# Performance work log

Hardware: AMD Instinct MI355X
Metric: run time of the kernel (lower is better)

## Reference

```python
import jax, jax.numpy as jnp
import numpy as np

N_NODES = 100000
N_EDGES = 1600000
D = 64
L = 3


def setup_inputs() -> dict:
    key = jax.random.key(0)
    ks = jax.random.split(key, 6)
    x = jax.random.normal(ks[0], (N_NODES, D), dtype=jnp.float32)
    edge_index = jax.random.randint(ks[1], (2, N_EDGES), 0, N_NODES, dtype=jnp.int64)
    # Stacked SAGEConv params: lin_l (neighbor branch, with bias), lin_r (root branch, no bias)
    scale = 1.0 / np.sqrt(D)
    Wl = jax.random.normal(ks[2], (L, D, D), dtype=jnp.float32) * scale
    bl = jnp.zeros((L, D), dtype=jnp.float32)
    Wr = jax.random.normal(ks[3], (L, D, D), dtype=jnp.float32) * scale
    return {
        "x": x,
        "Wl": Wl,
        "bl": bl,
        "Wr": Wr,
        "edge_index": edge_index,
        "batch_size": N_NODES,
        "framework": 1,
    }


def reference(x, Wl, bl, Wr, edge_index, batch_size, framework):
    src, dst = edge_index[0], edge_index[1]
    n = x.shape[0]
    # in-degree for mean aggregation; isolated nodes -> divide by 1 (result stays 0)
    deg = jax.ops.segment_sum(jnp.ones((src.shape[0],), dtype=x.dtype), dst, num_segments=n)
    inv_deg = (1.0 / jnp.maximum(deg, 1.0))[:, None]  # [N,1]
    for i in range(Wl.shape[0]):
        msg = x[src]                                              # [E, D] gather
        agg = jax.ops.segment_sum(msg, dst, num_segments=n) * inv_deg  # [N, D] mean
        x = jax.nn.relu(agg @ Wl[i].T + bl[i] + x @ Wr[i].T)
    if framework:
        return x
    return x[:batch_size]
```

## Files before the change

### kernel.cpp

```cpp
#include <hip/hip_runtime.h>
#include <hip/hip_bf16.h>


#define D 64
#define KDIM 128
#define TS 64
#define ASTH 144
#define BSH 9
#define BNODES 512
#define ECHUNK 4096
#define BCAP 12288

typedef unsigned long long u64;
typedef unsigned short u16;

__device__ inline u16 f2bf(float f) {
    unsigned u = __float_as_uint(f);
    return (u16)((u + 0x7fffu + ((u >> 16) & 1u)) >> 16);
}
__device__ inline void bfx8_to_f(uint4 u, float* f) {
    f[0] = __uint_as_float(u.x << 16); f[1] = __uint_as_float(u.x & 0xffff0000u);
    f[2] = __uint_as_float(u.y << 16); f[3] = __uint_as_float(u.y & 0xffff0000u);
    f[4] = __uint_as_float(u.z << 16); f[5] = __uint_as_float(u.z & 0xffff0000u);
    f[6] = __uint_as_float(u.w << 16); f[7] = __uint_as_float(u.w & 0xffff0000u);
}


__global__ __launch_bounds__(256) void convert_x_kernel(
    const float* __restrict__ x, u16* __restrict__ xb, int total8)
{
    int i = blockIdx.x * 256 + threadIdx.x;
    if (i >= total8) return;
    float4 a = *(const float4*)(x + (size_t)i * 8);
    float4 b = *(const float4*)(x + (size_t)i * 8 + 4);
    uint4 o;
    o.x = (unsigned)f2bf(a.x) | ((unsigned)f2bf(a.y) << 16);
    o.y = (unsigned)f2bf(a.z) | ((unsigned)f2bf(a.w) << 16);
    o.z = (unsigned)f2bf(b.x) | ((unsigned)f2bf(b.y) << 16);
    o.w = (unsigned)f2bf(b.z) | ((unsigned)f2bf(b.w) << 16);
    *(uint4*)(xb + (size_t)i * 8) = o;
}


__global__ __launch_bounds__(256) void bin_kernel(
    const int* __restrict__ srcp, const int* __restrict__ dstp,
    int* __restrict__ bcnt, u64* __restrict__ staging,
    int nE, int nb)
{
    __shared__ int hist[1024];
    __shared__ int bbase[1024];
    int t = threadIdx.x;
    int e0 = blockIdx.x * ECHUNK;
    for (int i = t; i < nb; i += 256) hist[i] = 0;
    __syncthreads();
    int dcache[16];
#pragma unroll
    for (int j = 0; j < 16; ++j) {
        int e = e0 + j * 256 + t;
        int d = (e < nE) ? dstp[e] : -1;
        dcache[j] = d;
        if (d >= 0) atomicAdd(&hist[d >> BSH], 1);
    }
    __syncthreads();
    for (int i = t; i < nb; i += 256) {
        int c = hist[i];
        bbase[i] = (c > 0) ? atomicAdd(&bcnt[i], c) : 0;
        hist[i] = 0;
    }
    __syncthreads();
#pragma unroll
    for (int j = 0; j < 16; ++j) {
        int e = e0 + j * 256 + t;
        int d = dcache[j];
        if (d >= 0) {
            int b = d >> BSH;
            int pos = bbase[b] + atomicAdd(&hist[b], 1);
            u64 rec = ((u64)(unsigned)(d & (BNODES - 1)) << 32) | (unsigned)srcp[e];
            staging[(size_t)b * BCAP + pos] = rec;
        }
    }
}

__global__ __launch_bounds__(64) void scan_bcnt_kernel(
    const int* __restrict__ bcnt, int* __restrict__ bbase, int nb)
{
    int lane = threadIdx.x;
    int carry = 0;
    for (int base = 0; base < nb; base += 64) {
        int i = base + lane;
        int v = (i < nb) ? bcnt[i] : 0;
        int inc = v;
#pragma unroll
        for (int off = 1; off < 64; off <<= 1) {
            int v2 = __shfl_up(inc, off);
            if (lane >= off) inc += v2;
        }
        if (i < nb) bbase[i] = carry + (inc - v);
        carry += __shfl(inc, 63);
    }
}

__global__ __launch_bounds__(256) void bucket_build_kernel(
    const u64* __restrict__ staging, const int* __restrict__ bcnt,
    const int* __restrict__ bbase, int* __restrict__ offs,
    float* __restrict__ inv, int* __restrict__ csr, int n, int nb, int E)
{
    __shared__ int hist[BNODES];
    __shared__ int loffs[BNODES + 1];
    __shared__ int cur[BNODES];
    int b = blockIdx.x, t = threadIdx.x;
    int n0 = b << BSH;
    int nodes = min(BNODES, n - n0);
    int cnt = bcnt[b];
    int gbase = bbase[b];
    const u64* seg = staging + (size_t)b * BCAP;
    for (int i = t; i < nodes; i += 256) { hist[i] = 0; cur[i] = 0; }
    __syncthreads();
    for (int e = t; e < cnt; e += 256) atomicAdd(&hist[(int)(seg[e] >> 32)], 1);
    __syncthreads();
    if (t < 64) {
        int carry = 0;
        for (int base0 = 0; base0 < nodes; base0 += 64) {
            int i = base0 + t;
            int v = (i < nodes) ? hist[i] : 0;
            int inc = v;
#pragma unroll
            for (int off = 1; off < 64; off <<= 1) {
                int v2 = __shfl_up(inc, off);
                if (t >= off) inc += v2;
            }
            if (i < nodes) loffs[i] = carry + (inc - v);
            carry += __shfl(inc, 63);
        }
        if (t == 0) loffs[nodes] = carry;
    }
    __syncthreads();
    for (int i = t; i < nodes; i += 256) {
        offs[n0 + i] = gbase + loffs[i];
        inv[n0 + i] = 1.0f / fmaxf((float)hist[i], 1.0f);
    }
    if (b == nb - 1 && t == 0) offs[n] = E;
    for (int e = t; e < cnt; e += 256) {
        u64 rec = seg[e];
        int dl = (int)(rec >> 32);
        int sv = (int)(rec & 0xffffffffu);
        int pos = loffs[dl] + atomicAdd(&cur[dl], 1);
        csr[gbase + pos] = sv;
    }
}

__global__ void transpose_w_kernel(const float* __restrict__ Wl,
                                   const float* __restrict__ Wr,
                                   float* __restrict__ WT, int total)
{
    int idx = blockIdx.x * 256 + threadIdx.x;
    if (idx >= total) return;
    int j = idx & 63;
    int k = (idx >> 6) & (KDIM - 1);
    int l = idx >> 13;
    float v = (k < D) ? Wl[((l * D) + j) * D + k]
                      : Wr[((l * D) + j) * D + (k - D)];
    WT[idx] = v;
}


template <int WRITE_F32>
__global__ __launch_bounds__(256) void layer_kernel(
    const u16* __restrict__ xin, const int* __restrict__ offs,
    const int* __restrict__ csr, const float* __restrict__ inv,
    const float* __restrict__ WT,
    const float* __restrict__ bl,
    void* __restrict__ outp, int n)
{
    __shared__ u16 A[TS * ASTH];
    const int t = threadIdx.x, w = t >> 6, lane = t & 63;
    const int sub = lane >> 3;
    const int fl  = lane & 7;
    const int base = lane & 56;
    const int v0 = blockIdx.x * TS;

#pragma unroll
    for (int g = 0; g < 2; ++g) {
        const int r = w * 16 + g * 8 + sub;
        const int v = v0 + r;
        int s = 0, e = 0;
        float scale = 0.f;
        uint4 xv = make_uint4(0, 0, 0, 0);
        if (v < n) {
            s = offs[v];
            e = offs[v + 1];
            scale = inv[v];
            xv = *(const uint4*)(xin + (size_t)v * D + fl * 8);
        }
        float acc[8] = {};
        while (__any(s < e)) {
            int idx = 0;
            if (s + fl < e) idx = csr[s + fl];
            int cnt = e - s;
            cnt = cnt < 0 ? 0 : (cnt > 8 ? 8 : cnt);
            int idxv[8];
#pragma unroll
            for (int j = 0; j < 8; ++j) idxv[j] = __shfl(idx, base + j);
            uint4 rows[8];
#pragma unroll
            for (int j = 0; j < 8; ++j)
                rows[j] = *(const uint4*)(xin + (size_t)idxv[j] * D + fl * 8);
#pragma unroll
            for (int j = 0; j < 8; ++j) {
                float f[8];
                bfx8_to_f(rows[j], f);
                float m = (j < cnt) ? 1.f : 0.f;
#pragma unroll
                for (int q = 0; q < 8; ++q) acc[q] = fmaf(f[q], m, acc[q]);
            }
            s += 8;
        }
        uint4 o;
        o.x = (unsigned)f2bf(acc[0] * scale) | ((unsigned)f2bf(acc[1] * scale) << 16);
        o.y = (unsigned)f2bf(acc[2] * scale) | ((unsigned)f2bf(acc[3] * scale) << 16);
        o.z = (unsigned)f2bf(acc[4] * scale) | ((unsigned)f2bf(acc[5] * scale) << 16);
        o.w = (unsigned)f2bf(acc[6] * scale) | ((unsigned)f2bf(acc[7] * scale) << 16);
        *(uint4*)(&A[r * ASTH + fl * 8]) = o;
        *(uint4*)(&A[r * ASTH + D + fl * 8]) = xv;
    }
    __syncthreads();

    const int c = (t & 15) * 4;
    const int r = (t >> 4) * 4;
    float acc[4][4] = {};
    for (int k = 0; k < KDIM; k += 8) {
        float4 b[8];
#pragma unroll
        for (int kk = 0; kk < 8; ++kk)
            b[kk] = *(const float4*)(WT + (k + kk) * D + c);
#pragma unroll
        for (int rr = 0; rr < 4; ++rr) {
            uint4 au = *(const uint4*)(&A[(r + rr) * ASTH + k]);
            float a[8];
            bfx8_to_f(au, a);
#pragma unroll
            for (int kk = 0; kk < 8; ++kk) {
                acc[rr][0] = fmaf(a[kk], b[kk].x, acc[rr][0]);
                acc[rr][1] = fmaf(a[kk], b[kk].y, acc[rr][1]);
                acc[rr][2] = fmaf(a[kk], b[kk].z, acc[rr][2]);
                acc[rr][3] = fmaf(a[kk], b[kk].w, acc[rr][3]);
            }
        }
    }

    float4 bias = *(const float4*)(bl + c);
#pragma unroll
    for (int rr = 0; rr < 4; ++rr) {
        int v = v0 + r + rr;
        if (v < n) {
            float o0 = fmaxf(acc[rr][0] + bias.x, 0.f);
            float o1 = fmaxf(acc[rr][1] + bias.y, 0.f);
            float o2 = fmaxf(acc[rr][2] + bias.z, 0.f);
            float o3 = fmaxf(acc[rr][3] + bias.w, 0.f);
            if (WRITE_F32) {
                *(float4*)((float*)outp + (size_t)v * D + c) = make_float4(o0, o1, o2, o3);
            } else {
                uint2 p;
                p.x = (unsigned)f2bf(o0) | ((unsigned)f2bf(o1) << 16);
                p.y = (unsigned)f2bf(o2) | ((unsigned)f2bf(o3) << 16);
                *(uint2*)((u16*)outp + (size_t)v * D + c) = p;
            }
        }
    }
}


extern "C" void kernel_launch(void* const* d_in, const int* in_sizes, int n_in,
                              void* d_out, int out_size, void* d_ws, size_t ws_size,
                              hipStream_t stream)
{
    const float* x  = (const float*)d_in[0];
    const float* Wl = (const float*)d_in[1];
    const float* bl = (const float*)d_in[2];
    const float* Wr = (const float*)d_in[3];
    const int*   ei = (const int*)d_in[4];

    const int N = in_sizes[0] / D;
    const int E = in_sizes[4] / 2;
    const int L = in_sizes[1] / (D * D);

    const int* srcp = ei;
    const int* dstp = ei + E;

    const int nbuck = (N + BNODES - 1) >> BSH;

    char* w = (char*)d_ws;
    int* bcnt  = (int*)w;               w += 1024 * sizeof(int);
    int* bbase = (int*)w;               w += 1024 * sizeof(int);
    int* offs  = (int*)w;               w += (size_t)(N + 1) * sizeof(int);
    w = (char*)(((uintptr_t)w + 15) & ~(uintptr_t)15);
    float* inv = (float*)w;             w += (size_t)N * sizeof(float);
    w = (char*)(((uintptr_t)w + 15) & ~(uintptr_t)15);
    int* csr   = (int*)w;               w += (size_t)E * sizeof(int);
    w = (char*)(((uintptr_t)w + 15) & ~(uintptr_t)15);
    float* wt  = (float*)w;             w += (size_t)L * KDIM * D * sizeof(float);
    w = (char*)(((uintptr_t)w + 15) & ~(uintptr_t)15);
    u16* xbf0  = (u16*)w;               w += (size_t)N * D * sizeof(u16);
    w = (char*)(((uintptr_t)w + 15) & ~(uintptr_t)15);
    u16* xbf1  = (u16*)w;               w += (size_t)N * D * sizeof(u16);
    w = (char*)(((uintptr_t)w + 15) & ~(uintptr_t)15);
    u16* xbf2  = (u16*)w;               w += (size_t)N * D * sizeof(u16);
    w = (char*)(((uintptr_t)w + 15) & ~(uintptr_t)15);
    u64* staging = (u64*)w;

    hipMemsetAsync(bcnt, 0, 1024 * sizeof(int), stream);

    convert_x_kernel<<<(N * D / 8 + 255) / 256, 256, 0, stream>>>(x, xbf0, N * D / 8);
    bin_kernel<<<(E + ECHUNK - 1) / ECHUNK, 256, 0, stream>>>(srcp, dstp, bcnt, staging, E, nbuck);
    scan_bcnt_kernel<<<1, 64, 0, stream>>>(bcnt, bbase, nbuck);
    bucket_build_kernel<<<nbuck, 256, 0, stream>>>(staging, bcnt, bbase, offs, inv, csr, N, nbuck, E);

    int wtotal = L * KDIM * D;
    transpose_w_kernel<<<(wtotal + 255) / 256, 256, 0, stream>>>(Wl, Wr, wt, wtotal);

    const int nblk = (N + TS - 1) / TS;
    const u16* xcur = xbf0;
    for (int i = 0; i < L; ++i) {
        const float* WTl = wt + (size_t)i * KDIM * D;
        const float* bll = bl + (size_t)i * D;
        if (i == L - 1) {
            layer_kernel<1><<<nblk, 256, 0, stream>>>(xcur, offs, csr, inv, WTl, bll, d_out, N);
        } else {
            u16* xdst = (i & 1) ? xbf2 : xbf1;
            layer_kernel<0><<<nblk, 256, 0, stream>>>(xcur, offs, csr, inv, WTl, bll, xdst, N);
            xcur = xdst;
        }
    }
}
```

Before: 350.5 us.

## Use bf16 MFMA for layer GEMM and interleave two-node gather loops

Replaces the scalar FP32 FMA GEMM in the layer kernel with 16x16x32 bf16 MFMA instructions, using weights prepacked into bf16 fragment order by a new pack kernel. The neighbor gather now runs both node groups in one loop so more independent row loads are in flight per iteration. The LDS row stride is reduced. Weights are now rounded to bf16, which costs some precision. Output stores become scalar per element instead of vectorized.

```diff
diff --git a/kernel.cpp b/kernel.cpp
--- a/kernel.cpp
+++ b/kernel.cpp
@@ -5,7 +5,7 @@
 #define D 64
 #define KDIM 128
 #define TS 64
-#define ASTH 144
+#define ASTH 136
 #define BSH 9
 #define BNODES 512
 #define ECHUNK 4096
@@ -13,6 +13,8 @@
 
 typedef unsigned long long u64;
 typedef unsigned short u16;
+typedef __attribute__((ext_vector_type(8))) short bf16x8;
+typedef __attribute__((ext_vector_type(4))) float f32x4;
 
 __device__ inline u16 f2bf(float f) {
     unsigned u = __float_as_uint(f);
@@ -149,18 +151,22 @@
     }
 }
 
-__global__ void transpose_w_kernel(const float* __restrict__ Wl,
-                                   const float* __restrict__ Wr,
-                                   float* __restrict__ WT, int total)
+__global__ void pack_w_kernel(const float* __restrict__ Wl,
+                              const float* __restrict__ Wr,
+                              u16* __restrict__ wpk, int total)
 {
     int idx = blockIdx.x * 256 + threadIdx.x;
     if (idx >= total) return;
-    int j = idx & 63;
-    int k = (idx >> 6) & (KDIM - 1);
-    int l = idx >> 13;
-    float v = (k < D) ? Wl[((l * D) + j) * D + k]
-                      : Wr[((l * D) + j) * D + (k - D)];
-    WT[idx] = v;
+    int j    = idx & 7;
+    int lane = (idx >> 3) & 63;
+    int nt   = (idx >> 9) & 3;
+    int kt   = (idx >> 11) & 3;
+    int l    = idx >> 13;
+    int k = kt * 32 + (lane >> 4) * 8 + j;
+    int n = nt * 16 + (lane & 15);
+    float v = (k < D) ? Wl[((l * D) + n) * D + k]
+                      : Wr[((l * D) + n) * D + (k - D)];
+    wpk[idx] = f2bf(v);
 }
 
 
@@ -168,7 +174,7 @@
 __global__ __launch_bounds__(256) void layer_kernel(
     const u16* __restrict__ xin, const int* __restrict__ offs,
     const int* __restrict__ csr, const float* __restrict__ inv,
-    const float* __restrict__ WT,
+    const u16* __restrict__ wpk,
     const float* __restrict__ bl,
     void* __restrict__ outp, int n)
 {
@@ -179,91 +185,97 @@
     const int base = lane & 56;
     const int v0 = blockIdx.x * TS;
 
+    int s[2], e[2];
+    float scale[2];
+    uint4 xv[2];
+    float acc[2][8] = {};
+#pragma unroll
+    for (int g = 0; g < 2; ++g) {
+        const int v = v0 + w * 16 + g * 8 + sub;
+        s[g] = 0; e[g] = 0; scale[g] = 0.f;
+        xv[g] = make_uint4(0, 0, 0, 0);
+        if (v < n) {
+            s[g] = offs[v];
+            e[g] = offs[v + 1];
+            scale[g] = inv[v];
+            xv[g] = *(const uint4*)(xin + (size_t)v * D + fl * 8);
+        }
+    }
+    while (__any((s[0] < e[0]) | (s[1] < e[1]))) {
+        int idx0 = 0, idx1 = 0;
+        if (s[0] + fl < e[0]) idx0 = csr[s[0] + fl];
+        if (s[1] + fl < e[1]) idx1 = csr[s[1] + fl];
+        int c0 = e[0] - s[0]; c0 = c0 < 0 ? 0 : (c0 > 8 ? 8 : c0);
+        int c1 = e[1] - s[1]; c1 = c1 < 0 ? 0 : (c1 > 8 ? 8 : c1);
+        int iv0[8], iv1[8];
+#pragma unroll
+        for (int j = 0; j < 8; ++j) iv0[j] = __shfl(idx0, base + j);
+#pragma unroll
+        for (int j = 0; j < 8; ++j) iv1[j] = __shfl(idx1, base + j);
+        uint4 rows0[8], rows1[8];
+#pragma unroll
+        for (int j = 0; j < 8; ++j)
+            rows0[j] = *(const uint4*)(xin + (size_t)iv0[j] * D + fl * 8);
+#pragma unroll
+        for (int j = 0; j < 8; ++j)
+            rows1[j] = *(const uint4*)(xin + (size_t)iv1[j] * D + fl * 8);
+#pragma unroll
+        for (int j = 0; j < 8; ++j) {
+            float f[8];
+            bfx8_to_f(rows0[j], f);
+            float m = (j < c0) ? 1.f : 0.f;
+#pragma unroll
+            for (int q = 0; q < 8; ++q) acc[0][q] = fmaf(f[q], m, acc[0][q]);
+        }
+#pragma unroll
+        for (int j = 0; j < 8; ++j) {
+            float f[8];
+            bfx8_to_f(rows1[j], f);
+            float m = (j < c1) ? 1.f : 0.f;
+#pragma unroll
+            for (int q = 0; q < 8; ++q) acc[1][q] = fmaf(f[q], m, acc[1][q]);
+        }
+        s[0] += 8; s[1] += 8;
+    }
 #pragma unroll
     for (int g = 0; g < 2; ++g) {
         const int r = w * 16 + g * 8 + sub;
-        const int v = v0 + r;
-        int s = 0, e = 0;
-        float scale = 0.f;
-        uint4 xv = make_uint4(0, 0, 0, 0);
-        if (v < n) {
-            s = offs[v];
-            e = offs[v + 1];
-            scale = inv[v];
-            xv = *(const uint4*)(xin + (size_t)v * D + fl * 8);
-        }
-        float acc[8] = {};
-        while (__any(s < e)) {
-            int idx = 0;
-            if (s + fl < e) idx = csr[s + fl];
-            int cnt = e - s;
-            cnt = cnt < 0 ? 0 : (cnt > 8 ? 8 : cnt);
-            int idxv[8];
-#pragma unroll
-            for (int j = 0; j < 8; ++j) idxv[j] = __shfl(idx, base + j);
-            uint4 rows[8];
-#pragma unroll
-            for (int j = 0; j < 8; ++j)
-                rows[j] = *(const uint4*)(xin + (size_t)idxv[j] * D + fl * 8);
-#pragma unroll
-            for (int j = 0; j < 8; ++j) {
-                float f[8];
-                bfx8_to_f(rows[j], f);
-                float m = (j < cnt) ? 1.f : 0.f;
-#pragma unroll
-                for (int q = 0; q < 8; ++q) acc[q] = fmaf(f[q], m, acc[q]);
-            }
-            s += 8;
-        }
         uint4 o;
-        o.x = (unsigned)f2bf(acc[0] * scale) | ((unsigned)f2bf(acc[1] * scale) << 16);
-        o.y = (unsigned)f2bf(acc[2] * scale) | ((unsigned)f2bf(acc[3] * scale) << 16);
-        o.z = (unsigned)f2bf(acc[4] * scale) | ((unsigned)f2bf(acc[5] * scale) << 16);
-        o.w = (unsigned)f2bf(acc[6] * scale) | ((unsigned)f2bf(acc[7] * scale) << 16);
+        o.x = (unsigned)f2bf(acc[g][0] * scale[g]) | ((unsigned)f2bf(acc[g][1] * scale[g]) << 16);
+        o.y = (unsigned)f2bf(acc[g][2] * scale[g]) | ((unsigned)f2bf(acc[g][3] * scale[g]) << 16);
+        o.z = (unsigned)f2bf(acc[g][4] * scale[g]) | ((unsigned)f2bf(acc[g][5] * scale[g]) << 16);
+        o.w = (unsigned)f2bf(acc[g][6] * scale[g]) | ((unsigned)f2bf(acc[g][7] * scale[g]) << 16);
         *(uint4*)(&A[r * ASTH + fl * 8]) = o;
-        *(uint4*)(&A[r * ASTH + D + fl * 8]) = xv;
-    }
-    __syncthreads();
-
-    const int c = (t & 15) * 4;
-    const int r = (t >> 4) * 4;
-    float acc[4][4] = {};
-    for (int k = 0; k < KDIM; k += 8) {
-        float4 b[8];
-#pragma unroll
-        for (int kk = 0; kk < 8; ++kk)
-            b[kk] = *(const float4*)(WT + (k + kk) * D + c);
-#pragma unroll
-        for (int rr = 0; rr < 4; ++rr) {
-            uint4 au = *(const uint4*)(&A[(r + rr) * ASTH + k]);
-            float a[8];
-            bfx8_to_f(au, a);
-#pragma unroll
-            for (int kk = 0; kk < 8; ++kk) {
-                acc[rr][0] = fmaf(a[kk], b[kk].x, acc[rr][0]);
-                acc[rr][1] = fmaf(a[kk], b[kk].y, acc[rr][1]);
-                acc[rr][2] = fmaf(a[kk], b[kk].z, acc[rr][2]);
-                acc[rr][3] = fmaf(a[kk], b[kk].w, acc[rr][3]);
-            }
-        }
-    }
-
-    float4 bias = *(const float4*)(bl + c);
-#pragma unroll
-    for (int rr = 0; rr < 4; ++rr) {
-        int v = v0 + r + rr;
-        if (v < n) {
-            float o0 = fmaxf(acc[rr][0] + bias.x, 0.f);
-            float o1 = fmaxf(acc[rr][1] + bias.y, 0.f);
-            float o2 = fmaxf(acc[rr][2] + bias.z, 0.f);
-            float o3 = fmaxf(acc[rr][3] + bias.w, 0.f);
-            if (WRITE_F32) {
-                *(float4*)((float*)outp + (size_t)v * D + c) = make_float4(o0, o1, o2, o3);
-            } else {
-                uint2 p;
-                p.x = (unsigned)f2bf(o0) | ((unsigned)f2bf(o1) << 16);
-                p.y = (unsigned)f2bf(o2) | ((unsigned)f2bf(o3) << 16);
-                *(uint2*)((u16*)outp + (size_t)v * D + c) = p;
+        *(uint4*)(&A[r * ASTH + D + fl * 8]) = xv[g];
+    }
+    __syncthreads();
+
+    const int m = lane & 15, quad = lane >> 4;
+    f32x4 cacc[4];
+#pragma unroll
+    for (int nt = 0; nt < 4; ++nt) cacc[nt] = (f32x4){0.f, 0.f, 0.f, 0.f};
+#pragma unroll
+    for (int kt = 0; kt < 4; ++kt) {
+        bf16x8 af = *(const bf16x8*)(&A[(w * 16 + m) * ASTH + kt * 32 + quad * 8]);
+#pragma unroll
+        for (int nt = 0; nt < 4; ++nt) {
+            bf16x8 bf = *(const bf16x8*)(wpk + (size_t)((kt * 4 + nt) * 64 + lane) * 8);
+            cacc[nt] = __builtin_amdgcn_mfma_f32_16x16x32_bf16(af, bf, cacc[nt], 0, 0, 0);
+        }
+    }
+#pragma unroll
+    for (int nt = 0; nt < 4; ++nt) {
+        float bias = bl[nt * 16 + m];
+#pragma unroll
+        for (int reg = 0; reg < 4; ++reg) {
+            int row = w * 16 + quad * 4 + reg;
+            int v = v0 + row;
+            if (v < n) {
+                float val = fmaxf(cacc[nt][reg] + bias, 0.f);
+                if (WRITE_F32)
+                    ((float*)outp)[(size_t)v * D + nt * 16 + m] = val;
+                else
+                    ((u16*)outp)[(size_t)v * D + nt * 16 + m] = f2bf(val);
             }
         }
     }
@@ -298,7 +310,7 @@
     w = (char*)(((uintptr_t)w + 15) & ~(uintptr_t)15);
     int* csr   = (int*)w;               w += (size_t)E * sizeof(int);
     w = (char*)(((uintptr_t)w + 15) & ~(uintptr_t)15);
-    float* wt  = (float*)w;             w += (size_t)L * KDIM * D * sizeof(float);
+    u16* wpk   = (u16*)w;               w += (size_t)L * 8192 * sizeof(u16);
     w = (char*)(((uintptr_t)w + 15) & ~(uintptr_t)15);
     u16* xbf0  = (u16*)w;               w += (size_t)N * D * sizeof(u16);
     w = (char*)(((uintptr_t)w + 15) & ~(uintptr_t)15);
@@ -315,19 +327,19 @@
     scan_bcnt_kernel<<<1, 64, 0, stream>>>(bcnt, bbase, nbuck);
     bucket_build_kernel<<<nbuck, 256, 0, stream>>>(staging, bcnt, bbase, offs, inv, csr, N, nbuck, E);
 
-    int wtotal = L * KDIM * D;
-    transpose_w_kernel<<<(wtotal + 255) / 256, 256, 0, stream>>>(Wl, Wr, wt, wtotal);
+    int wtotal = L * 8192;
+    pack_w_kernel<<<(wtotal + 255) / 256, 256, 0, stream>>>(Wl, Wr, wpk, wtotal);
 
     const int nblk = (N + TS - 1) / TS;
     const u16* xcur = xbf0;
     for (int i = 0; i < L; ++i) {
-        const float* WTl = wt + (size_t)i * KDIM * D;
+        const u16* wpl = wpk + (size_t)i * 8192;
         const float* bll = bl + (size_t)i * D;
         if (i == L - 1) {
-            layer_kernel<1><<<nblk, 256, 0, stream>>>(xcur, offs, csr, inv, WTl, bll, d_out, N);
+            layer_kernel<1><<<nblk, 256, 0, stream>>>(xcur, offs, csr, inv, wpl, bll, d_out, N);
         } else {
             u16* xdst = (i & 1) ? xbf2 : xbf1;
-            layer_kernel<0><<<nblk, 256, 0, stream>>>(xcur, offs, csr, inv, WTl, bll, xdst, N);
+            layer_kernel<0><<<nblk, 256, 0, stream>>>(xcur, offs, csr, inv, wpl, bll, xdst, N);
             xcur = xdst;
         }
     }
```

After: 324.3 us. -7.5%, faster.
